# Kernel tuning notes

Hardware: AMD Instinct MI355X
Metric: run time of the kernel (lower is better)

Reference implementation:

```python
import math
import jax, jax.numpy as jnp
import numpy as np

WS = 16        # window size (square)
SHIFT = 8      # window_size // 2 (window_shift=True)
NUM_HEADS = 6

def _rel_coords_table(ws):
    # Swin-V2 log-spaced continuous relative coords, shape (1, 2ws-1, 2ws-1, 2)
    r = np.arange(-(ws - 1), ws, dtype=np.float32)
    t = np.stack(np.meshgrid(r, r, indexing='ij'), axis=-1)[None]
    t = t / (ws - 1) * 8.0
    t = np.sign(t) * np.log2(np.abs(t) + 1.0) / np.log2(8.0)
    return t.astype(np.float32)

def _rel_pos_index(ws):
    ch, cw = np.meshgrid(np.arange(ws), np.arange(ws), indexing='ij')
    coords = np.stack([ch.ravel(), cw.ravel()])          # (2, N)
    rel = coords[:, :, None] - coords[:, None, :]        # (2, N, N)
    rel = rel.transpose(1, 2, 0).astype(np.int64)
    rel[..., 0] += ws - 1
    rel[..., 1] += ws - 1
    rel[..., 0] *= 2 * ws - 1
    return rel.sum(-1).astype(np.int32)                  # (N, N), values in [0, (2ws-1)^2)

def _shift_mask(H, W, ws, shift):
    img = np.zeros((H, W), dtype=np.float32)
    cnt = 0
    for hs in (slice(0, -ws), slice(-ws, -shift), slice(-shift, None)):
        for wsl in (slice(0, -ws), slice(-ws, -shift), slice(-shift, None)):
            img[hs, wsl] = cnt; cnt += 1
    win = img.reshape(H // ws, ws, W // ws, ws).transpose(0, 2, 1, 3).reshape(-1, ws * ws)
    diff = win[:, None, :] - win[:, :, None]
    return np.where(diff != 0, -100.0, 0.0).astype(np.float32)  # (nW, N, N)

def setup_inputs():
    key = jax.random.key(0)
    ks = jax.random.split(key, 4)
    B, H, W = 16, 64, 64
    C = 3 * NUM_HEADS * 32  # 576 (qkv channels)
    qkv = jax.random.normal(ks[0], (B, H * W, C), dtype=jnp.float32)
    table = jnp.asarray(_rel_coords_table(WS))
    index = jnp.asarray(_rel_pos_index(WS))
    mask = jnp.asarray(_shift_mask(H, W, WS, SHIFT))
    logit_scale = jnp.log(10.0 * jnp.ones((NUM_HEADS, 1, 1), dtype=jnp.float32))
    w1 = jax.random.normal(ks[1], (512, 2), dtype=jnp.float32) * 0.02
    b1 = jnp.zeros((512,), dtype=jnp.float32)
    w2 = jax.random.normal(ks[2], (NUM_HEADS, 512), dtype=jnp.float32) * 0.02
    return {"qkv": qkv, "table": table, "mask": mask, "logit_scale": logit_scale,
            "w1": w1, "b1": b1, "w2": w2, "index": index, "H": H, "W": W}

def reference(qkv, table, mask, logit_scale, w1, b1, w2, index, H, W):
    B, L, C = qkv.shape
    dim = C // 3
    hd = dim // NUM_HEADS
    x = qkv.reshape(B, H, W, C)
    x = jnp.roll(x, (-SHIFT, -SHIFT), axis=(1, 2))
    nWh, nWw = H // WS, W // WS
    # window partition -> (B_, N, C)
    x = x.reshape(B, nWh, WS, nWw, WS, C).transpose(0, 1, 3, 2, 4, 5).reshape(-1, WS * WS, C)
    B_, N, _ = x.shape
    qkv_ = x.reshape(B_, N, 3, NUM_HEADS, hd).transpose(2, 0, 3, 1, 4)
    q, k, v = qkv_[0], qkv_[1], qkv_[2]  # (B_, H, N, hd)
    # cosine attention
    qn = q / jnp.maximum(jnp.linalg.norm(q, axis=-1, keepdims=True), 1e-12)
    kn = k / jnp.maximum(jnp.linalg.norm(k, axis=-1, keepdims=True), 1e-12)
    attn = jnp.einsum('bhnd,bhmd->bhnm', qn, kn)
    scale = jnp.exp(jnp.minimum(logit_scale, math.log(1.0 / 0.01)))  # (H,1,1)
    attn = attn * scale[None]
    # CPB MLP bias: Linear(2,512)+ReLU -> Linear(512,H,no bias)
    hidden = jax.nn.relu(table @ w1.T + b1)          # (1, 2ws-1, 2ws-1, 512)
    bias_table = (hidden @ w2.T).reshape(-1, NUM_HEADS)
    bias = bias_table[index.reshape(-1)].reshape(N, N, NUM_HEADS).transpose(2, 0, 1)
    attn = attn + 16.0 * jax.nn.sigmoid(bias)[None]
    # shifted-window mask
    nWm = mask.shape[0]
    attn = attn.reshape(B_ // nWm, nWm, NUM_HEADS, N, N) + mask[None, :, None]
    attn = attn.reshape(B_, NUM_HEADS, N, N)
    attn = jax.nn.softmax(attn, axis=-1)
    out = jnp.einsum('bhnm,bhmd->bhnd', attn, v)
    out = out.transpose(0, 2, 1, 3).reshape(B_, N, dim)
    # window reverse + unshift
    out = out.reshape(B, nWh, nWw, WS, WS, dim).transpose(0, 1, 3, 2, 4, 5).reshape(B, H, W, dim)
    out = jnp.roll(out, (SHIFT, SHIFT), axis=(1, 2))
    return out.reshape(B, L, dim)
```

## Files before the change

kernel.cpp:

```cpp
#include <hip/hip_runtime.h>
#include <cstdint>

#define NH 6
#define HD 32
#define NTOK 256
#define CIN 576
#define DIMO 192
#define LOG2E 1.44269504f
#define SHIFT2 37.6f
#define MNEG (-144.269504f)

typedef short short8 __attribute__((ext_vector_type(8)));
typedef float f32x4 __attribute__((ext_vector_type(4)));
typedef int   int4v __attribute__((ext_vector_type(4)));

__device__ __forceinline__ int grp6(int x) { return (x < 48) ? 0 : ((x < 56) ? 1 : 2); }

__device__ __forceinline__ unsigned short f2bf(float f) {
    unsigned int u = __float_as_uint(f);
    u += 0x7fffu + ((u >> 16) & 1u);
    return (unsigned short)(u >> 16);
}

__device__ __forceinline__ int qk_off(int tile, int row, int quad) {
    return tile * 512 + row * 32 + ((quad ^ ((row >> 1) & 3)) << 3);
}

__global__ void cpb_kernel(const float* __restrict__ table,
                           const float* __restrict__ w1,
                           const float* __restrict__ b1,
                           const float* __restrict__ w2,
                           float* __restrict__ bv) {
    __shared__ float hid[512];
    int p = blockIdx.x;
    float t0 = table[2 * p], t1 = table[2 * p + 1];
    int t = threadIdx.x;
    for (int j = t; j < 512; j += 256) {
        float hv = fmaf(t0, w1[2 * j], fmaf(t1, w1[2 * j + 1], b1[j]));
        hid[j] = fmaxf(hv, 0.f);
    }
    __syncthreads();
    if (t < 192) {
        int h = t >> 5, l = t & 31;
        const float* w2h = w2 + h * 512;
        float acc = 0.f;
        for (int j = l; j < 512; j += 32) acc = fmaf(hid[j], w2h[j], acc);
        acc += __shfl_xor(acc, 1, 32);
        acc += __shfl_xor(acc, 2, 32);
        acc += __shfl_xor(acc, 4, 32);
        acc += __shfl_xor(acc, 8, 32);
        acc += __shfl_xor(acc, 16, 32);
        if (l == 0) bv[h * 961 + p] = (16.f / (1.f + __expf(-acc))) * LOG2E - SHIFT2;
    }
}

__global__ __launch_bounds__(512, 4) void attn_kernel(
    const float* __restrict__ qkv,
    const float* __restrict__ logit_scale,
    const float* __restrict__ bv,
    float* __restrict__ out)
{
    __shared__ __align__(16) short Qb[NTOK * HD];
    __shared__ __align__(16) short Kb[NTOK * HD];
    __shared__ __align__(16) short Vt[HD * 264];
    __shared__ float Bv[961];

    const int t = threadIdx.x;

    const int id  = blockIdx.x;
    const int r8  = id & 7, q3 = id >> 3;
    const int j24 = q3 % 24, g8 = q3 / 24;
    const int gg  = r8 + 8 * g8;
    const int h   = j24 % 6, ww = j24 / 6;
    const int wh  = gg & 3,  b  = gg >> 2;

    const float scale2 = __expf(fminf(logit_scale[h], 4.6051702f)) * LOG2E;

    for (int p = t; p < 961; p += 512) Bv[p] = bv[h * 961 + p];

    {
        const int n = t >> 1, s = t & 1;
        const int i = n >> 4, j = n & 15;
        const int rr = (wh * 16 + i + 8) & 63;
        const int cc = (ww * 16 + j + 8) & 63;
        const float* base = qkv + ((long)(b * 4096 + rr * 64 + cc)) * CIN + h * HD;

        float xv[32];
        {
            const float4* p4 = (const float4*)(base + s * DIMO);
#pragma unroll
            for (int w = 0; w < 8; ++w) {
                float4 x = p4[w];
                xv[4 * w + 0] = x.x; xv[4 * w + 1] = x.y; xv[4 * w + 2] = x.z; xv[4 * w + 3] = x.w;
            }
        }
        float vv[16];
        {
            const float4* v4 = (const float4*)(base + 2 * DIMO + s * 16);
#pragma unroll
            for (int w = 0; w < 4; ++w) {
                float4 x = v4[w];
                vv[4 * w + 0] = x.x; vv[4 * w + 1] = x.y; vv[4 * w + 2] = x.z; vv[4 * w + 3] = x.w;
            }
        }

        float a0 = 0.f, a1 = 0.f, a2 = 0.f, a3 = 0.f;
#pragma unroll
        for (int d = 0; d < 8; ++d) {
            a0 = fmaf(xv[d],      xv[d],      a0);
            a1 = fmaf(xv[d + 8],  xv[d + 8],  a1);
            a2 = fmaf(xv[d + 16], xv[d + 16], a2);
            a3 = fmaf(xv[d + 24], xv[d + 24], a3);
        }
        float ssum = (a0 + a1) + (a2 + a3);
        float sc = (s ? 1.f : scale2) / fmaxf(sqrtf(ssum), 1e-12f);

        short* dst = s ? Kb : Qb;
#pragma unroll
        for (int w = 0; w < 4; ++w) {
            short8 xc;
#pragma unroll
            for (int e = 0; e < 8; ++e) xc[e] = (short)f2bf(xv[8 * w + e] * sc);
            *(short8*)&dst[qk_off(i, j, w)] = xc;
        }

        {
            int u = (n >> 1) & 15;
            int jp = ((u & 1) << 3) | ((u & 2) << 1) | ((u & 4) >> 1) | ((u & 8) >> 3);
            int col = (n >> 5) * 32 + 2 * jp + (n & 1);
#pragma unroll
            for (int di = 0; di < 16; ++di) {
                int e = (di + 4 * s) & 15;
                Vt[(s * 16 + e) * 264 + col] = (short)f2bf(vv[e]);
            }
        }
    }
    __syncthreads();

    const int wv = t >> 6, lane = t & 63, quad = lane >> 4, l15 = lane & 15;

    int trg[2] = {wv * 2, wv * 2 + 1};
    short8 bQ[2];
#pragma unroll
    for (int tl = 0; tl < 2; ++tl)
        bQ[tl] = *(const short8*)&Qb[qk_off(trg[tl], l15, quad)];

    int gqr[2];
#pragma unroll
    for (int tl = 0; tl < 2; ++tl) gqr[tl] = grp6(wh * 16 + trg[tl]);
    const int gcl = grp6(ww * 16 + l15);
    float cm[4];
#pragma unroll
    for (int reg = 0; reg < 4; ++reg)
        cm[reg] = (gcl == grp6(ww * 16 + quad * 4 + reg)) ? 0.f : MNEG;

    f32x4 O[2][2];
    float lp[2] = {0.f, 0.f};
#pragma unroll
    for (int tl = 0; tl < 2; ++tl)
#pragma unroll
        for (int dtk = 0; dtk < 2; ++dtk) O[tl][dtk] = (f32x4){0.f, 0.f, 0.f, 0.f};

    const f32x4 Zero = (f32x4){0.f, 0.f, 0.f, 0.f};

    for (int c = 0; c < 8; ++c) {
        int ctg[2] = {2 * c, 2 * c + 1};
        short8 aK[2], bV[2];
#pragma unroll
        for (int ct = 0; ct < 2; ++ct)
            aK[ct] = *(const short8*)&Kb[qk_off(ctg[ct], l15, quad)];
#pragma unroll
        for (int dtk = 0; dtk < 2; ++dtk)
            bV[dtk] = *(const short8*)&Vt[(dtk * 16 + l15) * 264 + c * 32 + quad * 8];

        f32x4 S[2][2];
#pragma unroll
        for (int tl = 0; tl < 2; ++tl)
#pragma unroll
            for (int ct = 0; ct < 2; ++ct)
                S[tl][ct] = __builtin_amdgcn_mfma_f32_16x16x32_bf16(aK[ct], bQ[tl], Zero, 0, 0, 0);

        int gkr[2] = {grp6(wh * 16 + ctg[0]), grp6(wh * 16 + ctg[1])};

#pragma unroll
        for (int tl = 0; tl < 2; ++tl) {
            float ev[2][4];
#pragma unroll
            for (int ct = 0; ct < 2; ++ct) {
                int rb = (trg[tl] - ctg[ct] + 15) * 31 + 15 + l15 - 4 * quad;
                bool rmatch = (gqr[tl] == gkr[ct]);
#pragma unroll
                for (int reg = 0; reg < 4; ++reg) {
                    float madd = rmatch ? cm[reg] : MNEG;
                    float arg = S[tl][ct][reg] + (Bv[rb - reg] + madd);
                    float e = __builtin_amdgcn_exp2f(arg);
                    ev[ct][reg] = e;
                    lp[tl] += e;
                }
            }
            int p0, p1, p2, p3;
            asm("v_cvt_pk_bf16_f32 %0, %1, %2" : "=v"(p0) : "v"(ev[0][0]), "v"(ev[0][1]));
            asm("v_cvt_pk_bf16_f32 %0, %1, %2" : "=v"(p1) : "v"(ev[1][0]), "v"(ev[1][1]));
            asm("v_cvt_pk_bf16_f32 %0, %1, %2" : "=v"(p2) : "v"(ev[0][2]), "v"(ev[0][3]));
            asm("v_cvt_pk_bf16_f32 %0, %1, %2" : "=v"(p3) : "v"(ev[1][2]), "v"(ev[1][3]));
            asm("v_permlane32_swap_b32 %0, %1" : "+v"(p0), "+v"(p2));
            asm("v_permlane32_swap_b32 %0, %1" : "+v"(p1), "+v"(p3));
            int4v w = {p0, p1, p2, p3};
            union { int4v i; short8 s; } cvt; cvt.i = w;
            short8 aP = cvt.s;
            O[tl][0] = __builtin_amdgcn_mfma_f32_16x16x32_bf16(aP, bV[0], O[tl][0], 0, 0, 0);
            O[tl][1] = __builtin_amdgcn_mfma_f32_16x16x32_bf16(aP, bV[1], O[tl][1], 0, 0, 0);
        }
    }

    const long pixb = (long)b * 4096;
#pragma unroll
    for (int tl = 0; tl < 2; ++tl) {
        float s = lp[tl];
        s += __shfl_xor(s, 16);
        s += __shfl_xor(s, 32);
        float invf = 1.f / s;
        int r = (wh * 16 + trg[tl] + 8) & 63;
#pragma unroll
        for (int reg = 0; reg < 4; ++reg) {
            float iv = __shfl(invf, quad * 4 + reg);
            int cpix = (ww * 16 + quad * 4 + reg + 8) & 63;
            float* op = out + (pixb + r * 64 + cpix) * DIMO + h * HD + l15;
            op[0]  = O[tl][0][reg] * iv;
            op[16] = O[tl][1][reg] * iv;
        }
    }
}

extern "C" void kernel_launch(void* const* d_in, const int* in_sizes, int n_in,
                              void* d_out, int out_size, void* d_ws, size_t ws_size,
                              hipStream_t stream) {
    const float* qkv         = (const float*)d_in[0];
    const float* table       = (const float*)d_in[1];
    const float* logit_scale = (const float*)d_in[3];
    const float* w1          = (const float*)d_in[4];
    const float* b1          = (const float*)d_in[5];
    const float* w2          = (const float*)d_in[6];
    float* out = (float*)d_out;
    float* bv  = (float*)d_ws;

    cpb_kernel<<<961, 256, 0, stream>>>(table, w1, b1, w2, bv);
    attn_kernel<<<256 * NH, 512, 0, stream>>>(qkv, logit_scale, bv, out);
}
```

Baseline: 262.7 us.

## Make attention kernel persistent over three windows with Q/K prefetch

Shrinks the attention grid from 1536 to 512 blocks, each looping over three (window, head) work items. While computing one item, the block prefetches the next item's Q/K rows from global memory into registers, so load latency overlaps with MFMA and softmax work. The trade-off is higher register pressure, an extra barrier per iteration, and fewer blocks to spread load across CUs.

```diff
diff --git a/kernel.cpp b/kernel.cpp
--- a/kernel.cpp
+++ b/kernel.cpp
@@ -24,6 +24,19 @@
 
 __device__ __forceinline__ int qk_off(int tile, int row, int quad) {
     return tile * 512 + row * 32 + ((quad ^ ((row >> 1) & 3)) << 3);
+}
+
+struct Win { int b, wh, ww, h; };
+__device__ __forceinline__ Win decode_win(int id) {
+    int r8 = id & 7, q3 = id >> 3;
+    int j24 = q3 % 24, g8 = q3 / 24;
+    int gg = r8 + 8 * g8;
+    Win w;
+    w.h  = j24 % 6;
+    w.ww = j24 / 6;
+    w.wh = gg & 3;
+    w.b  = gg >> 2;
+    return w;
 }
 
 __global__ void cpb_kernel(const float* __restrict__ table,
@@ -66,65 +79,72 @@
     __shared__ float Bv[961];
 
     const int t = threadIdx.x;
-
-    const int id  = blockIdx.x;
-    const int r8  = id & 7, q3 = id >> 3;
-    const int j24 = q3 % 24, g8 = q3 / 24;
-    const int gg  = r8 + 8 * g8;
-    const int h   = j24 % 6, ww = j24 / 6;
-    const int wh  = gg & 3,  b  = gg >> 2;
-
-    const float scale2 = __expf(fminf(logit_scale[h], 4.6051702f)) * LOG2E;
-
-    for (int p = t; p < 961; p += 512) Bv[p] = bv[h * 961 + p];
-
+    const int n = t >> 1, s = t & 1;
+    const int i = n >> 4, j = n & 15;
+    const int wv = t >> 6, lane = t & 63, quad = lane >> 4, l15 = lane & 15;
+    const int trg0 = wv * 2, trg1 = wv * 2 + 1;
+
+    Win W = decode_win(blockIdx.x);
+
+    float4 pq[8];
     {
-        const int n = t >> 1, s = t & 1;
-        const int i = n >> 4, j = n & 15;
+        const int rr = (W.wh * 16 + i + 8) & 63;
+        const int cc = (W.ww * 16 + j + 8) & 63;
+        const float4* p4 = (const float4*)(qkv + ((long)(W.b * 4096 + rr * 64 + cc)) * CIN + W.h * HD + s * DIMO);
+#pragma unroll
+        for (int w = 0; w < 8; ++w) pq[w] = p4[w];
+    }
+
+#pragma unroll 1
+    for (int it = 0; it < 3; ++it) {
+        const int b = W.b, wh = W.wh, ww = W.ww, h = W.h;
+        const float scale2 = __expf(fminf(logit_scale[h], 4.6051702f)) * LOG2E;
+
         const int rr = (wh * 16 + i + 8) & 63;
         const int cc = (ww * 16 + j + 8) & 63;
         const float* base = qkv + ((long)(b * 4096 + rr * 64 + cc)) * CIN + h * HD;
 
-        float xv[32];
-        {
-            const float4* p4 = (const float4*)(base + s * DIMO);
-#pragma unroll
-            for (int w = 0; w < 8; ++w) {
-                float4 x = p4[w];
-                xv[4 * w + 0] = x.x; xv[4 * w + 1] = x.y; xv[4 * w + 2] = x.z; xv[4 * w + 3] = x.w;
-            }
-        }
-        float vv[16];
+        float4 vr[4];
         {
             const float4* v4 = (const float4*)(base + 2 * DIMO + s * 16);
 #pragma unroll
+            for (int w = 0; w < 4; ++w) vr[w] = v4[w];
+        }
+        for (int q = t; q < 961; q += 512) Bv[q] = bv[h * 961 + q];
+
+        {
+            float xv[32];
+#pragma unroll
+            for (int w = 0; w < 8; ++w) {
+                xv[4 * w + 0] = pq[w].x; xv[4 * w + 1] = pq[w].y;
+                xv[4 * w + 2] = pq[w].z; xv[4 * w + 3] = pq[w].w;
+            }
+            float a0 = 0.f, a1 = 0.f, a2 = 0.f, a3 = 0.f;
+#pragma unroll
+            for (int d = 0; d < 8; ++d) {
+                a0 = fmaf(xv[d],      xv[d],      a0);
+                a1 = fmaf(xv[d + 8],  xv[d + 8],  a1);
+                a2 = fmaf(xv[d + 16], xv[d + 16], a2);
+                a3 = fmaf(xv[d + 24], xv[d + 24], a3);
+            }
+            float ssum = (a0 + a1) + (a2 + a3);
+            float sc = (s ? 1.f : scale2) / fmaxf(sqrtf(ssum), 1e-12f);
+            short* dst = s ? Kb : Qb;
+#pragma unroll
             for (int w = 0; w < 4; ++w) {
-                float4 x = v4[w];
-                vv[4 * w + 0] = x.x; vv[4 * w + 1] = x.y; vv[4 * w + 2] = x.z; vv[4 * w + 3] = x.w;
-            }
-        }
-
-        float a0 = 0.f, a1 = 0.f, a2 = 0.f, a3 = 0.f;
-#pragma unroll
-        for (int d = 0; d < 8; ++d) {
-            a0 = fmaf(xv[d],      xv[d],      a0);
-            a1 = fmaf(xv[d + 8],  xv[d + 8],  a1);
-            a2 = fmaf(xv[d + 16], xv[d + 16], a2);
-            a3 = fmaf(xv[d + 24], xv[d + 24], a3);
-        }
-        float ssum = (a0 + a1) + (a2 + a3);
-        float sc = (s ? 1.f : scale2) / fmaxf(sqrtf(ssum), 1e-12f);
-
-        short* dst = s ? Kb : Qb;
-#pragma unroll
-        for (int w = 0; w < 4; ++w) {
-            short8 xc;
-#pragma unroll
-            for (int e = 0; e < 8; ++e) xc[e] = (short)f2bf(xv[8 * w + e] * sc);
-            *(short8*)&dst[qk_off(i, j, w)] = xc;
-        }
-
+                short8 xc;
+#pragma unroll
+                for (int e = 0; e < 8; ++e) xc[e] = (short)f2bf(xv[8 * w + e] * sc);
+                *(short8*)&dst[qk_off(i, j, w)] = xc;
+            }
+        }
         {
+            float vv[16];
+#pragma unroll
+            for (int w = 0; w < 4; ++w) {
+                vv[4 * w + 0] = vr[w].x; vv[4 * w + 1] = vr[w].y;
+                vv[4 * w + 2] = vr[w].z; vv[4 * w + 3] = vr[w].w;
+            }
             int u = (n >> 1) & 15;
             int jp = ((u & 1) << 3) | ((u & 2) << 1) | ((u & 4) >> 1) | ((u & 8) >> 3);
             int col = (n >> 5) * 32 + 2 * jp + (n & 1);
@@ -134,100 +154,104 @@
                 Vt[(s * 16 + e) * 264 + col] = (short)f2bf(vv[e]);
             }
         }
-    }
-    __syncthreads();
-
-    const int wv = t >> 6, lane = t & 63, quad = lane >> 4, l15 = lane & 15;
-
-    int trg[2] = {wv * 2, wv * 2 + 1};
-    short8 bQ[2];
-#pragma unroll
-    for (int tl = 0; tl < 2; ++tl)
-        bQ[tl] = *(const short8*)&Qb[qk_off(trg[tl], l15, quad)];
-
-    int gqr[2];
-#pragma unroll
-    for (int tl = 0; tl < 2; ++tl) gqr[tl] = grp6(wh * 16 + trg[tl]);
-    const int gcl = grp6(ww * 16 + l15);
-    float cm[4];
-#pragma unroll
-    for (int reg = 0; reg < 4; ++reg)
-        cm[reg] = (gcl == grp6(ww * 16 + quad * 4 + reg)) ? 0.f : MNEG;
-
-    f32x4 O[2][2];
-    float lp[2] = {0.f, 0.f};
-#pragma unroll
-    for (int tl = 0; tl < 2; ++tl)
-#pragma unroll
-        for (int dtk = 0; dtk < 2; ++dtk) O[tl][dtk] = (f32x4){0.f, 0.f, 0.f, 0.f};
-
-    const f32x4 Zero = (f32x4){0.f, 0.f, 0.f, 0.f};
-
-    for (int c = 0; c < 8; ++c) {
-        int ctg[2] = {2 * c, 2 * c + 1};
-        short8 aK[2], bV[2];
-#pragma unroll
-        for (int ct = 0; ct < 2; ++ct)
-            aK[ct] = *(const short8*)&Kb[qk_off(ctg[ct], l15, quad)];
-#pragma unroll
-        for (int dtk = 0; dtk < 2; ++dtk)
-            bV[dtk] = *(const short8*)&Vt[(dtk * 16 + l15) * 264 + c * 32 + quad * 8];
-
-        f32x4 S[2][2];
+        __syncthreads();
+
+        if (it < 2) {
+            Win Wn = decode_win(blockIdx.x + 512 * (it + 1));
+            const int rr2 = (Wn.wh * 16 + i + 8) & 63;
+            const int cc2 = (Wn.ww * 16 + j + 8) & 63;
+            const float4* p4 = (const float4*)(qkv + ((long)(Wn.b * 4096 + rr2 * 64 + cc2)) * CIN + Wn.h * HD + s * DIMO);
+#pragma unroll
+            for (int w = 0; w < 8; ++w) pq[w] = p4[w];
+            W = Wn;
+        }
+        __builtin_amdgcn_sched_barrier(0);
+
+        short8 bQ[2];
+        bQ[0] = *(const short8*)&Qb[qk_off(trg0, l15, quad)];
+        bQ[1] = *(const short8*)&Qb[qk_off(trg1, l15, quad)];
+
+        const int gqr[2] = {grp6(wh * 16 + trg0), grp6(wh * 16 + trg1)};
+        const int gcl = grp6(ww * 16 + l15);
+        float cm[4];
+#pragma unroll
+        for (int reg = 0; reg < 4; ++reg)
+            cm[reg] = (gcl == grp6(ww * 16 + quad * 4 + reg)) ? 0.f : MNEG;
+
+        f32x4 O[2][2];
+        float lp[2] = {0.f, 0.f};
 #pragma unroll
         for (int tl = 0; tl < 2; ++tl)
 #pragma unroll
+            for (int dtk = 0; dtk < 2; ++dtk) O[tl][dtk] = (f32x4){0.f, 0.f, 0.f, 0.f};
+
+        const f32x4 Zero = (f32x4){0.f, 0.f, 0.f, 0.f};
+        const int trg[2] = {trg0, trg1};
+
+        for (int c = 0; c < 8; ++c) {
+            int ctg[2] = {2 * c, 2 * c + 1};
+            short8 aK[2], bV[2];
+#pragma unroll
             for (int ct = 0; ct < 2; ++ct)
-                S[tl][ct] = __builtin_amdgcn_mfma_f32_16x16x32_bf16(aK[ct], bQ[tl], Zero, 0, 0, 0);
-
-        int gkr[2] = {grp6(wh * 16 + ctg[0]), grp6(wh * 16 + ctg[1])};
-
+                aK[ct] = *(const short8*)&Kb[qk_off(ctg[ct], l15, quad)];
+#pragma unroll
+            for (int dtk = 0; dtk < 2; ++dtk)
+                bV[dtk] = *(const short8*)&Vt[(dtk * 16 + l15) * 264 + c * 32 + quad * 8];
+
+            int gkr[2] = {grp6(wh * 16 + ctg[0]), grp6(wh * 16 + ctg[1])};
+
+#pragma unroll
+            for (int tl = 0; tl < 2; ++tl) {
+                f32x4 S0 = __builtin_amdgcn_mfma_f32_16x16x32_bf16(aK[0], bQ[tl], Zero, 0, 0, 0);
+                f32x4 S1 = __builtin_amdgcn_mfma_f32_16x16x32_bf16(aK[1], bQ[tl], Zero, 0, 0, 0);
+
+                float ev[2][4];
+#pragma unroll
+                for (int ct = 0; ct < 2; ++ct) {
+                    const f32x4& Sc = ct ? S1 : S0;
+                    int rb = (trg[tl] - ctg[ct] + 15) * 31 + 15 + l15 - 4 * quad;
+                    bool rmatch = (gqr[tl] == gkr[ct]);
+#pragma unroll
+                    for (int reg = 0; reg < 4; ++reg) {
+                        float madd = rmatch ? cm[reg] : MNEG;
+                        float arg = Sc[reg] + (Bv[rb - reg] + madd);
+                        float e = __builtin_amdgcn_exp2f(arg);
+                        ev[ct][reg] = e;
+                        lp[tl] += e;
+                    }
+                }
+                int p0, p1, p2, p3;
+                asm("v_cvt_pk_bf16_f32 %0, %1, %2" : "=v"(p0) : "v"(ev[0][0]), "v"(ev[0][1]));
+                asm("v_cvt_pk_bf16_f32 %0, %1, %2" : "=v"(p1) : "v"(ev[1][0]), "v"(ev[1][1]));
+                asm("v_cvt_pk_bf16_f32 %0, %1, %2" : "=v"(p2) : "v"(ev[0][2]), "v"(ev[0][3]));
+                asm("v_cvt_pk_bf16_f32 %0, %1, %2" : "=v"(p3) : "v"(ev[1][2]), "v"(ev[1][3]));
+                asm("v_permlane32_swap_b32 %0, %1" : "+v"(p0), "+v"(p2));
+                asm("v_permlane32_swap_b32 %0, %1" : "+v"(p1), "+v"(p3));
+                int4v wd = {p0, p1, p2, p3};
+                union { int4v iv; short8 sv; } cvt; cvt.iv = wd;
+                short8 aP = cvt.sv;
+                O[tl][0] = __builtin_amdgcn_mfma_f32_16x16x32_bf16(aP, bV[0], O[tl][0], 0, 0, 0);
+                O[tl][1] = __builtin_amdgcn_mfma_f32_16x16x32_bf16(aP, bV[1], O[tl][1], 0, 0, 0);
+            }
+        }
+        __syncthreads();
+
+        const long pixb = (long)b * 4096;
 #pragma unroll
         for (int tl = 0; tl < 2; ++tl) {
-            float ev[2][4];
-#pragma unroll
-            for (int ct = 0; ct < 2; ++ct) {
-                int rb = (trg[tl] - ctg[ct] + 15) * 31 + 15 + l15 - 4 * quad;
-                bool rmatch = (gqr[tl] == gkr[ct]);
-#pragma unroll
-                for (int reg = 0; reg < 4; ++reg) {
-                    float madd = rmatch ? cm[reg] : MNEG;
-                    float arg = S[tl][ct][reg] + (Bv[rb - reg] + madd);
-                    float e = __builtin_amdgcn_exp2f(arg);
-                    ev[ct][reg] = e;
-                    lp[tl] += e;
-                }
-            }
-            int p0, p1, p2, p3;
-            asm("v_cvt_pk_bf16_f32 %0, %1, %2" : "=v"(p0) : "v"(ev[0][0]), "v"(ev[0][1]));
-            asm("v_cvt_pk_bf16_f32 %0, %1, %2" : "=v"(p1) : "v"(ev[1][0]), "v"(ev[1][1]));
-            asm("v_cvt_pk_bf16_f32 %0, %1, %2" : "=v"(p2) : "v"(ev[0][2]), "v"(ev[0][3]));
-            asm("v_cvt_pk_bf16_f32 %0, %1, %2" : "=v"(p3) : "v"(ev[1][2]), "v"(ev[1][3]));
-            asm("v_permlane32_swap_b32 %0, %1" : "+v"(p0), "+v"(p2));
-            asm("v_permlane32_swap_b32 %0, %1" : "+v"(p1), "+v"(p3));
-            int4v w = {p0, p1, p2, p3};
-            union { int4v i; short8 s; } cvt; cvt.i = w;
-            short8 aP = cvt.s;
-            O[tl][0] = __builtin_amdgcn_mfma_f32_16x16x32_bf16(aP, bV[0], O[tl][0], 0, 0, 0);
-            O[tl][1] = __builtin_amdgcn_mfma_f32_16x16x32_bf16(aP, bV[1], O[tl][1], 0, 0, 0);
-        }
-    }
-
-    const long pixb = (long)b * 4096;
-#pragma unroll
-    for (int tl = 0; tl < 2; ++tl) {
-        float s = lp[tl];
-        s += __shfl_xor(s, 16);
-        s += __shfl_xor(s, 32);
-        float invf = 1.f / s;
-        int r = (wh * 16 + trg[tl] + 8) & 63;
-#pragma unroll
-        for (int reg = 0; reg < 4; ++reg) {
-            float iv = __shfl(invf, quad * 4 + reg);
-            int cpix = (ww * 16 + quad * 4 + reg + 8) & 63;
-            float* op = out + (pixb + r * 64 + cpix) * DIMO + h * HD + l15;
-            op[0]  = O[tl][0][reg] * iv;
-            op[16] = O[tl][1][reg] * iv;
+            float sm = lp[tl];
+            sm += __shfl_xor(sm, 16);
+            sm += __shfl_xor(sm, 32);
+            float invf = 1.f / sm;
+            int r = (wh * 16 + trg[tl] + 8) & 63;
+#pragma unroll
+            for (int reg = 0; reg < 4; ++reg) {
+                float iv = __shfl(invf, quad * 4 + reg);
+                int cpix = (ww * 16 + quad * 4 + reg + 8) & 63;
+                float* op = out + (pixb + r * 64 + cpix) * DIMO + h * HD + l15;
+                op[0]  = O[tl][0][reg] * iv;
+                op[16] = O[tl][1][reg] * iv;
+            }
         }
     }
 }
@@ -245,5 +269,5 @@
     float* bv  = (float*)d_ws;
 
     cpb_kernel<<<961, 256, 0, stream>>>(table, w1, b1, w2, bv);
-    attn_kernel<<<256 * NH, 512, 0, stream>>>(qkv, logit_scale, bv, out);
-}
+    attn_kernel<<<512, 512, 0, stream>>>(qkv, logit_scale, bv, out);
+}
```

Result: slower. 307.4 us (+17.0%).

## Load Q fragments directly from global into registers, drop Q shared buffer

Applied to the files above, without the earlier changes.

Removes the Q shared-memory tile. The staging pass now stores only per-token inverse norms for Q. Each wave reloads its own Q rows from global memory in MFMA fragment layout and scales and packs them to bf16 in registers. The change also raises the occupancy hint to 8 blocks per CU, reorders block indexing so all heads of a window are adjacent, and issues V loads before Q/K loads. These aim to cut LDS footprint and traffic and improve cache locality, at the cost of re-reading Q from global memory and more register pressure under the tighter launch bound.

```diff
diff --git a/kernel.cpp b/kernel.cpp
--- a/kernel.cpp
+++ b/kernel.cpp
@@ -54,25 +54,21 @@
     }
 }
 
-__global__ __launch_bounds__(512, 4) void attn_kernel(
+__global__ __launch_bounds__(512, 8) void attn_kernel(
     const float* __restrict__ qkv,
     const float* __restrict__ logit_scale,
     const float* __restrict__ bv,
     float* __restrict__ out)
 {
-    __shared__ __align__(16) short Qb[NTOK * HD];
     __shared__ __align__(16) short Kb[NTOK * HD];
     __shared__ __align__(16) short Vt[HD * 264];
     __shared__ float Bv[961];
+    __shared__ float Qn[NTOK];
 
     const int t = threadIdx.x;
-
-    const int id  = blockIdx.x;
-    const int r8  = id & 7, q3 = id >> 3;
-    const int j24 = q3 % 24, g8 = q3 / 24;
-    const int gg  = r8 + 8 * g8;
-    const int h   = j24 % 6, ww = j24 / 6;
-    const int wh  = gg & 3,  b  = gg >> 2;
+    const int h   = blockIdx.x % NH;
+    const int win = blockIdx.x / NH;
+    const int b = win >> 4, wl = win & 15, wh = wl >> 2, ww = wl & 3;
 
     const float scale2 = __expf(fminf(logit_scale[h], 4.6051702f)) * LOG2E;
 
@@ -85,6 +81,12 @@
         const int cc = (ww * 16 + j + 8) & 63;
         const float* base = qkv + ((long)(b * 4096 + rr * 64 + cc)) * CIN + h * HD;
 
+        float4 vr[4];
+        {
+            const float4* v4 = (const float4*)(base + 2 * DIMO + s * 16);
+#pragma unroll
+            for (int w = 0; w < 4; ++w) vr[w] = v4[w];
+        }
         float xv[32];
         {
             const float4* p4 = (const float4*)(base + s * DIMO);
@@ -94,16 +96,6 @@
                 xv[4 * w + 0] = x.x; xv[4 * w + 1] = x.y; xv[4 * w + 2] = x.z; xv[4 * w + 3] = x.w;
             }
         }
-        float vv[16];
-        {
-            const float4* v4 = (const float4*)(base + 2 * DIMO + s * 16);
-#pragma unroll
-            for (int w = 0; w < 4; ++w) {
-                float4 x = v4[w];
-                vv[4 * w + 0] = x.x; vv[4 * w + 1] = x.y; vv[4 * w + 2] = x.z; vv[4 * w + 3] = x.w;
-            }
-        }
-
         float a0 = 0.f, a1 = 0.f, a2 = 0.f, a3 = 0.f;
 #pragma unroll
         for (int d = 0; d < 8; ++d) {
@@ -113,18 +105,25 @@
             a3 = fmaf(xv[d + 24], xv[d + 24], a3);
         }
         float ssum = (a0 + a1) + (a2 + a3);
-        float sc = (s ? 1.f : scale2) / fmaxf(sqrtf(ssum), 1e-12f);
-
-        short* dst = s ? Kb : Qb;
-#pragma unroll
-        for (int w = 0; w < 4; ++w) {
-            short8 xc;
-#pragma unroll
-            for (int e = 0; e < 8; ++e) xc[e] = (short)f2bf(xv[8 * w + e] * sc);
-            *(short8*)&dst[qk_off(i, j, w)] = xc;
-        }
-
+        if (s == 0) {
+            Qn[n] = scale2 / fmaxf(sqrtf(ssum), 1e-12f);
+        } else {
+            float sc = 1.f / fmaxf(sqrtf(ssum), 1e-12f);
+#pragma unroll
+            for (int w = 0; w < 4; ++w) {
+                short8 xc;
+#pragma unroll
+                for (int e = 0; e < 8; ++e) xc[e] = (short)f2bf(xv[8 * w + e] * sc);
+                *(short8*)&Kb[qk_off(i, j, w)] = xc;
+            }
+        }
         {
+            float vv[16];
+#pragma unroll
+            for (int w = 0; w < 4; ++w) {
+                vv[4 * w + 0] = vr[w].x; vv[4 * w + 1] = vr[w].y;
+                vv[4 * w + 2] = vr[w].z; vv[4 * w + 3] = vr[w].w;
+            }
             int u = (n >> 1) & 15;
             int jp = ((u & 1) << 3) | ((u & 2) << 1) | ((u & 4) >> 1) | ((u & 8) >> 3);
             int col = (n >> 5) * 32 + 2 * jp + (n & 1);
@@ -135,19 +134,39 @@
             }
         }
     }
+
+    const int wv = t >> 6, lane = t & 63, quad = lane >> 4, l15 = lane & 15;
+    float4 qfa[2], qfb[2];
+#pragma unroll
+    for (int tl = 0; tl < 2; ++tl) {
+        int tok = wv * 32 + tl * 16 + l15;
+        int ii = tok >> 4, jj = tok & 15;
+        int rr2 = (wh * 16 + ii + 8) & 63;
+        int cc2 = (ww * 16 + jj + 8) & 63;
+        const float4* qp = (const float4*)(qkv + ((long)(b * 4096 + rr2 * 64 + cc2)) * CIN + h * HD + 8 * quad);
+        qfa[tl] = qp[0];
+        qfb[tl] = qp[1];
+    }
     __syncthreads();
 
-    const int wv = t >> 6, lane = t & 63, quad = lane >> 4, l15 = lane & 15;
-
-    int trg[2] = {wv * 2, wv * 2 + 1};
     short8 bQ[2];
 #pragma unroll
-    for (int tl = 0; tl < 2; ++tl)
-        bQ[tl] = *(const short8*)&Qb[qk_off(trg[tl], l15, quad)];
-
-    int gqr[2];
-#pragma unroll
-    for (int tl = 0; tl < 2; ++tl) gqr[tl] = grp6(wh * 16 + trg[tl]);
+    for (int tl = 0; tl < 2; ++tl) {
+        float qn = Qn[wv * 32 + tl * 16 + l15];
+        float f0 = qfa[tl].x * qn, f1 = qfa[tl].y * qn, f2 = qfa[tl].z * qn, f3 = qfa[tl].w * qn;
+        float f4 = qfb[tl].x * qn, f5 = qfb[tl].y * qn, f6 = qfb[tl].z * qn, f7 = qfb[tl].w * qn;
+        int d0, d1, d2, d3;
+        asm("v_cvt_pk_bf16_f32 %0, %1, %2" : "=v"(d0) : "v"(f0), "v"(f1));
+        asm("v_cvt_pk_bf16_f32 %0, %1, %2" : "=v"(d1) : "v"(f2), "v"(f3));
+        asm("v_cvt_pk_bf16_f32 %0, %1, %2" : "=v"(d2) : "v"(f4), "v"(f5));
+        asm("v_cvt_pk_bf16_f32 %0, %1, %2" : "=v"(d3) : "v"(f6), "v"(f7));
+        int4v wd = {d0, d1, d2, d3};
+        union { int4v iv; short8 sv; } cvt; cvt.iv = wd;
+        bQ[tl] = cvt.sv;
+    }
+
+    const int trg[2] = {wv * 2, wv * 2 + 1};
+    const int gqr[2] = {grp6(wh * 16 + trg[0]), grp6(wh * 16 + trg[1])};
     const int gcl = grp6(ww * 16 + l15);
     float cm[4];
 #pragma unroll
@@ -205,9 +224,9 @@
             asm("v_cvt_pk_bf16_f32 %0, %1, %2" : "=v"(p3) : "v"(ev[1][2]), "v"(ev[1][3]));
             asm("v_permlane32_swap_b32 %0, %1" : "+v"(p0), "+v"(p2));
             asm("v_permlane32_swap_b32 %0, %1" : "+v"(p1), "+v"(p3));
-            int4v w = {p0, p1, p2, p3};
-            union { int4v i; short8 s; } cvt; cvt.i = w;
-            short8 aP = cvt.s;
+            int4v wd = {p0, p1, p2, p3};
+            union { int4v iv; short8 sv; } cvt; cvt.iv = wd;
+            short8 aP = cvt.sv;
             O[tl][0] = __builtin_amdgcn_mfma_f32_16x16x32_bf16(aP, bV[0], O[tl][0], 0, 0, 0);
             O[tl][1] = __builtin_amdgcn_mfma_f32_16x16x32_bf16(aP, bV[1], O[tl][1], 0, 0, 0);
         }
```

Result: slower. 275.6 us (+4.9%).
